# Optimization experiments

Measured on AMD Instinct MI355X. Metric: run time of the kernel, lower is better.

Reference implementation:

```python
import jax, jax.numpy as jnp
import numpy as np

N = 100_000      # nodes
E = 3_200_000    # edges (before self-loops)
IN_DIM = 256
H1, H2 = 64, 32
OUT_DIM = 40
NEG_SLOPE = 0.2  # PyG GATConv default


def setup_inputs() -> dict:
    key = jax.random.key(0)
    ks = jax.random.split(key, 12)
    s = 0.05
    return {
        "x": jax.random.normal(ks[0], (N, IN_DIM), jnp.float32),
        "edge_index": jax.random.randint(ks[1], (2, E), 0, N, jnp.int32),
        "W1": jax.random.normal(ks[2], (IN_DIM, H1), jnp.float32) * s,
        "att_src1": jax.random.normal(ks[3], (H1,), jnp.float32) * s,
        "att_dst1": jax.random.normal(ks[4], (H1,), jnp.float32) * s,
        "b1": jnp.zeros((H1,), jnp.float32),
        "W2": jax.random.normal(ks[5], (H1, H2), jnp.float32) * s,
        "att_src2": jax.random.normal(ks[6], (H2,), jnp.float32) * s,
        "att_dst2": jax.random.normal(ks[7], (H2,), jnp.float32) * s,
        "b2": jnp.zeros((H2,), jnp.float32),
        "fcW": jax.random.normal(ks[8], (H2, OUT_DIM), jnp.float32) * s,
        "fcb": jnp.zeros((OUT_DIM,), jnp.float32),
    }


def gat_conv(x, src, dst, W, a_src, a_dst, b):
    """Single-head PyG GATConv (concat, heads=1). src/dst already include self-loops."""
    n = x.shape[0]
    h = x @ W                                   # [N, C] projected features (lin has no bias)
    alpha_s = (h * a_src).sum(-1)               # [N]
    alpha_d = (h * a_dst).sum(-1)               # [N]
    logit = jax.nn.leaky_relu(alpha_s[src] + alpha_d[dst], NEG_SLOPE)  # [E']
    # segment softmax over edges grouped by destination node
    m = jax.ops.segment_max(logit, dst, num_segments=n)               # [N]
    e = jnp.exp(logit - m[dst])                                        # [E']
    denom = jax.ops.segment_sum(e, dst, num_segments=n)               # [N]
    alpha = e / denom[dst]                                             # [E']
    out = jax.ops.segment_sum(h[src] * alpha[:, None], dst, num_segments=n)  # [N, C]
    return out + b


def reference(x, edge_index, W1, att_src1, att_dst1, b1, W2, att_src2, att_dst2, b2, fcW, fcb):
    n = x.shape[0]
    # add_self_loops=True (PyG GATConv default)
    loop = jnp.arange(n, dtype=edge_index.dtype)
    src = jnp.concatenate([edge_index[0], loop])
    dst = jnp.concatenate([edge_index[1], loop])
    h = jax.nn.relu(gat_conv(x, src, dst, W1, att_src1, att_dst1, b1))
    emb = jax.nn.relu(gat_conv(h, src, dst, W2, att_src2, att_dst2, b2))
    logits = emb @ fcW + fcb
    return emb, logits
```

## Files before the change

### kernel.cpp

```cpp
#include <hip/hip_runtime.h>
#include <hip/hip_bf16.h>

#define NEG_SLOPE 0.2f
#define IN_DIM 256
#define C1 64
#define C2 32
#define ODIM 40
#define SCAN_CHUNK 4096
#define BSHIFT 12
#define ECHUNK 8192
#define ECH2 16384
#define CH 10

typedef unsigned short ushort16;

__device__ __forceinline__ unsigned bf16_rne(float f) {
    unsigned a = __float_as_uint(f);
    return (a + 0x7FFFu + ((a >> 16) & 1u)) >> 16;
}
__device__ __forceinline__ void bf16x2_unpack(unsigned u, float& f0, float& f1) {
    f0 = __uint_as_float(u << 16);
    f1 = __uint_as_float(u & 0xFFFF0000u);
}


__global__ void k_bhist(const int* __restrict__ dst, int E, int* __restrict__ gh,
                        int nblk, int nb) {
    __shared__ int h[32];
    int t = threadIdx.x;
    if (t < 32) h[t] = 0;
    __syncthreads();
    int base = blockIdx.x * ECHUNK;
    int end = min(base + ECHUNK, E);
    for (int i = base + t; i < end; i += 256) atomicAdd(&h[dst[i] >> BSHIFT], 1);
    __syncthreads();
    if (t < nb) gh[t * nblk + blockIdx.x] = h[t];
}

__global__ void k_bscan(int* __restrict__ gh, int L) {
    __shared__ int lds[256];
    __shared__ int carry;
    int t = threadIdx.x;
    if (t == 0) carry = 0;
    __syncthreads();
    for (int base = 0; base < L; base += 256) {
        int v = (base + t < L) ? gh[base + t] : 0;
        lds[t] = v; __syncthreads();
        for (int off = 1; off < 256; off <<= 1) {
            int u = (t >= off) ? lds[t - off] : 0;
            __syncthreads();
            lds[t] += u;
            __syncthreads();
        }
        if (base + t < L) gh[base + t] = lds[t] - v + carry;
        __syncthreads();
        if (t == 0) carry += lds[255];
        __syncthreads();
    }
}

__global__ void k_bplace(const int* __restrict__ src, const int* __restrict__ dst, int E,
                         const int* __restrict__ gh, int nblk, int nb,
                         int2* __restrict__ pairs) {
    __shared__ int cur[32];
    int t = threadIdx.x;
    if (t < nb) cur[t] = gh[t * nblk + blockIdx.x];
    __syncthreads();
    int base = blockIdx.x * ECHUNK;
    int end = min(base + ECHUNK, E);
    for (int i = base + t; i < end; i += 256) {
        int d = dst[i];
        int pos = atomicAdd(&cur[d >> BSHIFT], 1);
        pairs[pos] = make_int2(src[i], d);
    }
}

__device__ __forceinline__ void bc_map(int blk, int* b, int* c) {
    int xcd = blk & 7, k = blk >> 3;
    *b = (k & 3) * 8 + xcd;
    *c = k >> 2;
}

__global__ __launch_bounds__(512)
void k_nhist(const int2* __restrict__ pairs, const int* __restrict__ gh, int nblk,
             int nb, int E, int* __restrict__ chist) {
    __shared__ int h[4096];
    int b, c; bc_map(blockIdx.x, &b, &c);
    if (b >= nb) return;
    for (int i = threadIdx.x; i < 4096; i += 512) h[i] = 0;
    __syncthreads();
    int estart = gh[b * nblk];
    int eend = (b + 1 < nb) ? gh[(b + 1) * nblk] : E;
    int s0 = estart + c * ECH2;
    int s1 = min(s0 + ECH2, eend);
    for (int i = s0 + threadIdx.x; i < s1; i += 512)
        atomicAdd(&h[pairs[i].y & 4095], 1);
    __syncthreads();
    int* out = chist + ((size_t)b * CH + c) * 4096;
    for (int i = threadIdx.x; i < 4096; i += 512) out[i] = h[i];
}

__global__ void k_cnt(const int* __restrict__ chist, int* __restrict__ cnt, int n) {
    int i = blockIdx.x * 256 + threadIdx.x;
    if (i >= n) return;
    int b = i >> BSHIFT, j = i & 4095;
    const int* p = chist + ((size_t)b * CH) * 4096 + j;
    int s = 1;
#pragma unroll
    for (int c = 0; c < CH; c++) s += p[c * 4096];
    cnt[i] = s;
}

__global__ void k_scan1(const int* __restrict__ cnt, int n, int* __restrict__ bsums) {
    __shared__ int lds[256];
    int t = threadIdx.x;
    int base = blockIdx.x * SCAN_CHUNK + t * 16;
    int s = 0;
#pragma unroll
    for (int i = 0; i < 16; i++) { int idx = base + i; s += (idx < n) ? cnt[idx] : 0; }
    lds[t] = s; __syncthreads();
    for (int off = 128; off > 0; off >>= 1) {
        if (t < off) lds[t] += lds[t + off];
        __syncthreads();
    }
    if (t == 0) bsums[blockIdx.x] = lds[0];
}

__global__ void k_scan2(int* bsums, int nb, int* row_ptr, int n, int total) {
    __shared__ int lds[256];
    int t = threadIdx.x;
    int v = (t < nb) ? bsums[t] : 0;
    lds[t] = v; __syncthreads();
    for (int off = 1; off < 256; off <<= 1) {
        int u = (t >= off) ? lds[t - off] : 0;
        __syncthreads();
        lds[t] += u;
        __syncthreads();
    }
    if (t < nb) bsums[t] = lds[t] - v;
    if (t == 0) row_ptr[n] = total;
}

__global__ void k_scan3(const int* __restrict__ cnt, int n, const int* __restrict__ bsums,
                        int* __restrict__ row_ptr) {
    __shared__ int lds[256];
    int t = threadIdx.x;
    int base = blockIdx.x * SCAN_CHUNK + t * 16;
    int loc[16];
    int s = 0;
#pragma unroll
    for (int i = 0; i < 16; i++) {
        int idx = base + i;
        int c = (idx < n) ? cnt[idx] : 0;
        loc[i] = s; s += c;
    }
    lds[t] = s; __syncthreads();
    for (int off = 1; off < 256; off <<= 1) {
        int u = (t >= off) ? lds[t - off] : 0;
        __syncthreads();
        lds[t] += u;
        __syncthreads();
    }
    int texcl = lds[t] - s + bsums[blockIdx.x];
#pragma unroll
    for (int i = 0; i < 16; i++) {
        int idx = base + i;
        if (idx < n) row_ptr[idx] = texcl + loc[i];
    }
}

__global__ void k_selfloop(const int* __restrict__ row_ptr, int n, int* __restrict__ adj) {
    int i = blockIdx.x * 256 + threadIdx.x;
    if (i < n) adj[row_ptr[i]] = i;
}

__global__ void k_nscan(int* __restrict__ chist, const int* __restrict__ row_ptr, int n) {
    int i = blockIdx.x * 256 + threadIdx.x;
    if (i >= n) return;
    int b = i >> BSHIFT, j = i & 4095;
    int* p = chist + ((size_t)b * CH) * 4096 + j;
    int s = row_ptr[i] + 1;
#pragma unroll
    for (int c = 0; c < CH; c++) { int t = p[c * 4096]; p[c * 4096] = s; s += t; }
}

__global__ __launch_bounds__(512)
void k_place2(const int2* __restrict__ pairs, const int* __restrict__ gh, int nblk,
              int nb, int E, const int* __restrict__ chist, int* __restrict__ adj) {
    __shared__ int cur[4096];
    int b, c; bc_map(blockIdx.x, &b, &c);
    if (b >= nb) return;
    const int* cs = chist + ((size_t)b * CH + c) * 4096;
    for (int i = threadIdx.x; i < 4096; i += 512) cur[i] = cs[i];
    __syncthreads();
    int estart = gh[b * nblk];
    int eend = (b + 1 < nb) ? gh[(b + 1) * nblk] : E;
    int s0 = estart + c * ECH2;
    int s1 = min(s0 + ECH2, eend);
    for (int i = s0 + threadIdx.x; i < s1; i += 512) {
        int2 p = pairs[i];
        int pos = atomicAdd(&cur[p.y & 4095], 1);
        adj[pos] = p.x;
    }
}


__global__ __launch_bounds__(256, 4)
void k_gemm1(const float* __restrict__ x, const float* __restrict__ W1,
             const float* __restrict__ attS, const float* __restrict__ attD,
             ushort16* __restrict__ h1b, float* __restrict__ asP,
             float* __restrict__ adP, int n) {
    int t = threadIdx.x;
    int wave = t >> 6, lane = t & 63;
    int half = blockIdx.x & 1;
    int chalf = half * 32;
    int row = (blockIdx.x >> 1) * 256 + wave * 64 + lane;
    bool active = row < n;
    int rowc = active ? row : n - 1;
    const float4* xr = (const float4*)(x + (size_t)rowc * IN_DIM);

    float acc[32];
#pragma unroll
    for (int c = 0; c < 32; c++) acc[c] = 0.f;

#define FMA_K(XC, KK) { \
        const float* wk = wb + (KK) * C1; \
        _Pragma("unroll") \
        for (int c = 0; c < 32; c++) acc[c] = fmaf((XC), wk[c], acc[c]); }

    for (int k0 = 0; k0 < 16; k0++) {
        float4 xv0 = xr[k0 * 4 + 0];
        float4 xv1 = xr[k0 * 4 + 1];
        float4 xv2 = xr[k0 * 4 + 2];
        float4 xv3 = xr[k0 * 4 + 3];
        const float* wb = W1 + (size_t)(k0 * 16) * C1 + chalf;
        FMA_K(xv0.x, 0)  FMA_K(xv0.y, 1)  FMA_K(xv0.z, 2)  FMA_K(xv0.w, 3)
        FMA_K(xv1.x, 4)  FMA_K(xv1.y, 5)  FMA_K(xv1.z, 6)  FMA_K(xv1.w, 7)
        FMA_K(xv2.x, 8)  FMA_K(xv2.y, 9)  FMA_K(xv2.z, 10) FMA_K(xv2.w, 11)
        FMA_K(xv3.x, 12) FMA_K(xv3.y, 13) FMA_K(xv3.z, 14) FMA_K(xv3.w, 15)
    }
#undef FMA_K

    if (!active) return;
    float vs = 0.f, vd = 0.f;
#pragma unroll
    for (int c = 0; c < 32; c++) {
        vs = fmaf(acc[c], attS[chalf + c], vs);
        vd = fmaf(acc[c], attD[chalf + c], vd);
    }
    asP[half * n + row] = vs;
    adP[half * n + row] = vd;

    uint4* hp = (uint4*)((ushort16*)h1b + (size_t)row * C1 + chalf);
#pragma unroll
    for (int j = 0; j < 4; j++) {
        unsigned p0 = bf16_rne(acc[j*8+0]) | (bf16_rne(acc[j*8+1]) << 16);
        unsigned p1 = bf16_rne(acc[j*8+2]) | (bf16_rne(acc[j*8+3]) << 16);
        unsigned p2 = bf16_rne(acc[j*8+4]) | (bf16_rne(acc[j*8+5]) << 16);
        unsigned p3 = bf16_rne(acc[j*8+6]) | (bf16_rne(acc[j*8+7]) << 16);
        hp[j] = make_uint4(p0, p1, p2, p3);
    }
}

__global__ void k_alphaC(const float* __restrict__ asP, const float* __restrict__ adP,
                         float* __restrict__ as1, float* __restrict__ ad1, int n) {
    int i = blockIdx.x * 256 + threadIdx.x;
    if (i < n) {
        as1[i] = asP[i] + asP[(size_t)n + i];
        ad1[i] = adP[i] + adP[(size_t)n + i];
    }
}


__global__ __launch_bounds__(256)
void k_agg1(const ushort16* __restrict__ h1b, const float* __restrict__ as1,
            const float* __restrict__ ad1, const int* __restrict__ row_ptr,
            const int* __restrict__ adj, const float* __restrict__ b1,
            float* __restrict__ h1out, int n) {
    int wave = (blockIdx.x * 256 + threadIdx.x) >> 6;
    int lane = threadIdx.x & 63;
    if (wave >= n) return;
    int d = wave;
    int beg = row_ptr[d], end = row_ptr[d + 1];
    float adv = ad1[d];
    int g = lane >> 3, cq = lane & 7;
    float acc[8];
#pragma unroll
    for (int k = 0; k < 8; k++) acc[k] = 0.f;
    float dsum = 0.f;

#define AGG1_ROUND(E_) { \
        int se = __shfl(s, (E_)); \
        float we = __shfl(w, (E_)); \
        uint4 u = ((const uint4*)(h1b + (size_t)se * C1))[cq]; \
        float f0, f1; \
        bf16x2_unpack(u.x, f0, f1); acc[0]=fmaf(we,f0,acc[0]); acc[1]=fmaf(we,f1,acc[1]); \
        bf16x2_unpack(u.y, f0, f1); acc[2]=fmaf(we,f0,acc[2]); acc[3]=fmaf(we,f1,acc[3]); \
        bf16x2_unpack(u.z, f0, f1); acc[4]=fmaf(we,f0,acc[4]); acc[5]=fmaf(we,f1,acc[5]); \
        bf16x2_unpack(u.w, f0, f1); acc[6]=fmaf(we,f0,acc[6]); acc[7]=fmaf(we,f1,acc[7]); }

    for (int base = beg; base < end; base += 64) {
        int cnt = min(64, end - base);
        int s = d; float w = 0.f;
        if (lane < cnt) {
            s = adj[base + lane];
            float lg = as1[s] + adv;
            lg = lg > 0.f ? lg : NEG_SLOPE * lg;
            w = expf(lg);
            dsum += w;
        }
        int j = 0;
        for (; j + 32 <= cnt; j += 32) {
            AGG1_ROUND(j + g)
            AGG1_ROUND(j + 8 + g)
            AGG1_ROUND(j + 16 + g)
            AGG1_ROUND(j + 24 + g)
        }
        for (; j < cnt; j += 8) AGG1_ROUND(j + g)
    }
#undef AGG1_ROUND

#pragma unroll
    for (int off = 32; off > 0; off >>= 1) dsum += __shfl_xor(dsum, off);
#pragma unroll
    for (int off = 8; off <= 32; off <<= 1) {
#pragma unroll
        for (int k = 0; k < 8; k++) acc[k] += __shfl_xor(acc[k], off);
    }
    if (g == 0) {
        float inv = 1.f / dsum;
        float4 bv0 = ((const float4*)b1)[cq * 2];
        float4 bv1 = ((const float4*)b1)[cq * 2 + 1];
        float4 o0, o1;
        o0.x = acc[0] * inv + bv0.x; o0.x = o0.x > 0.f ? o0.x : 0.f;
        o0.y = acc[1] * inv + bv0.y; o0.y = o0.y > 0.f ? o0.y : 0.f;
        o0.z = acc[2] * inv + bv0.z; o0.z = o0.z > 0.f ? o0.z : 0.f;
        o0.w = acc[3] * inv + bv0.w; o0.w = o0.w > 0.f ? o0.w : 0.f;
        o1.x = acc[4] * inv + bv1.x; o1.x = o1.x > 0.f ? o1.x : 0.f;
        o1.y = acc[5] * inv + bv1.y; o1.y = o1.y > 0.f ? o1.y : 0.f;
        o1.z = acc[6] * inv + bv1.z; o1.z = o1.z > 0.f ? o1.z : 0.f;
        o1.w = acc[7] * inv + bv1.w; o1.w = o1.w > 0.f ? o1.w : 0.f;
        float4* op = (float4*)(h1out + (size_t)d * C1 + cq * 8);
        op[0] = o0; op[1] = o1;
    }
}


__global__ __launch_bounds__(256)
void k_gemm2(const float* __restrict__ h1out, const float* __restrict__ W2,
             const float* __restrict__ attS, const float* __restrict__ attD,
             ushort16* __restrict__ h2b, float* __restrict__ as2,
             float* __restrict__ ad2, int n) {
    __shared__ float w2t[C2 * 68];
    __shared__ float sAttS[C2], sAttD[C2];
    int t = threadIdx.x;
    for (int i = t; i < C1 * C2; i += 256) {
        int k = i >> 5, c = i & 31;
        w2t[c * 68 + k] = W2[i];
    }
    if (t < C2) { sAttS[t] = attS[t]; sAttD[t] = attD[t]; }
    __syncthreads();
    int wave = t >> 6, lane = t & 63;
    int col = lane & 31, half = lane >> 5;
    int rowbase = blockIdx.x * 32 + wave * 8;
    const float* wrow = &w2t[col * 68];
    for (int rr = 0; rr < 8; rr += 2) {
        int row = rowbase + rr + half;
        if (row >= n) return;
        float acc = 0.f;
#pragma unroll
        for (int k = 0; k < C1; k += 4) {
            float4 wv = *(const float4*)&wrow[k];
            float4 xv = *(const float4*)&h1out[(size_t)row * C1 + k];
            acc = fmaf(xv.x, wv.x, acc);
            acc = fmaf(xv.y, wv.y, acc);
            acc = fmaf(xv.z, wv.z, acc);
            acc = fmaf(xv.w, wv.w, acc);
        }
        h2b[(size_t)row * C2 + col] = (ushort16)bf16_rne(acc);
        float vs = acc * sAttS[col], vd = acc * sAttD[col];
#pragma unroll
        for (int off = 16; off > 0; off >>= 1) {
            vs += __shfl_xor(vs, off);
            vd += __shfl_xor(vd, off);
        }
        if (col == 0) { as2[row] = vs; ad2[row] = vd; }
    }
}


__global__ __launch_bounds__(256)
void k_agg2(const ushort16* __restrict__ h2b, const float* __restrict__ as2,
            const float* __restrict__ ad2, const int* __restrict__ row_ptr,
            const int* __restrict__ adj, const float* __restrict__ b2,
            float* __restrict__ emb, int n) {
    int wave = (blockIdx.x * 256 + threadIdx.x) >> 6;
    int lane = threadIdx.x & 63;
    if (wave >= n) return;
    int d = wave;
    int beg = row_ptr[d], end = row_ptr[d + 1];
    float adv = ad2[d];
    int g = lane >> 2, cq = lane & 3;
    float acc[8];
#pragma unroll
    for (int k = 0; k < 8; k++) acc[k] = 0.f;
    float dsum = 0.f;

#define AGG2_ROUND(E_) { \
        int se = __shfl(s, (E_)); \
        float we = __shfl(w, (E_)); \
        uint4 u = ((const uint4*)(h2b + (size_t)se * C2))[cq]; \
        float f0, f1; \
        bf16x2_unpack(u.x, f0, f1); acc[0]=fmaf(we,f0,acc[0]); acc[1]=fmaf(we,f1,acc[1]); \
        bf16x2_unpack(u.y, f0, f1); acc[2]=fmaf(we,f0,acc[2]); acc[3]=fmaf(we,f1,acc[3]); \
        bf16x2_unpack(u.z, f0, f1); acc[4]=fmaf(we,f0,acc[4]); acc[5]=fmaf(we,f1,acc[5]); \
        bf16x2_unpack(u.w, f0, f1); acc[6]=fmaf(we,f0,acc[6]); acc[7]=fmaf(we,f1,acc[7]); }

    for (int base = beg; base < end; base += 64) {
        int cnt = min(64, end - base);
        int s = d; float w = 0.f;
        if (lane < cnt) {
            s = adj[base + lane];
            float lg = as2[s] + adv;
            lg = lg > 0.f ? lg : NEG_SLOPE * lg;
            w = expf(lg);
            dsum += w;
        }
        int j = 0;
        for (; j + 64 <= cnt; j += 64) {
            AGG2_ROUND(j + g)
            AGG2_ROUND(j + 16 + g)
            AGG2_ROUND(j + 32 + g)
            AGG2_ROUND(j + 48 + g)
        }
        for (; j < cnt; j += 16) AGG2_ROUND(j + g)
    }
#undef AGG2_ROUND

#pragma unroll
    for (int off = 32; off > 0; off >>= 1) dsum += __shfl_xor(dsum, off);
#pragma unroll
    for (int off = 4; off <= 32; off <<= 1) {
#pragma unroll
        for (int k = 0; k < 8; k++) acc[k] += __shfl_xor(acc[k], off);
    }
    if (g == 0) {
        float inv = 1.f / dsum;
        float4 bv0 = ((const float4*)b2)[cq * 2];
        float4 bv1 = ((const float4*)b2)[cq * 2 + 1];
        float4 o0, o1;
        o0.x = acc[0] * inv + bv0.x; o0.x = o0.x > 0.f ? o0.x : 0.f;
        o0.y = acc[1] * inv + bv0.y; o0.y = o0.y > 0.f ? o0.y : 0.f;
        o0.z = acc[2] * inv + bv0.z; o0.z = o0.z > 0.f ? o0.z : 0.f;
        o0.w = acc[3] * inv + bv0.w; o0.w = o0.w > 0.f ? o0.w : 0.f;
        o1.x = acc[4] * inv + bv1.x; o1.x = o1.x > 0.f ? o1.x : 0.f;
        o1.y = acc[5] * inv + bv1.y; o1.y = o1.y > 0.f ? o1.y : 0.f;
        o1.z = acc[6] * inv + bv1.z; o1.z = o1.z > 0.f ? o1.z : 0.f;
        o1.w = acc[7] * inv + bv1.w; o1.w = o1.w > 0.f ? o1.w : 0.f;
        float4* op = (float4*)(emb + (size_t)d * C2 + cq * 8);
        op[0] = o0; op[1] = o1;
    }
}


__global__ __launch_bounds__(256)
void k_logits(const float* __restrict__ emb, const float* __restrict__ fcW,
              const float* __restrict__ fcb, float* __restrict__ out, int n) {
    __shared__ float w[C2 * ODIM];
    __shared__ float b[ODIM];
    int t = threadIdx.x;
    for (int i = t; i < C2 * ODIM; i += 256) w[i] = fcW[i];
    if (t < ODIM) b[t] = fcb[t];
    __syncthreads();
    int lane = t & 63;
    int row = blockIdx.x * 4 + (t >> 6);
    if (row >= n) return;
    float acc = (lane < ODIM) ? b[lane] : 0.f;
    const float4* er = (const float4*)&emb[(size_t)row * C2];
#pragma unroll
    for (int c4 = 0; c4 < 8; c4++) {
        float4 e = er[c4];
        int c = c4 * 4;
        if (lane < ODIM) {
            acc = fmaf(e.x, w[(c + 0) * ODIM + lane], acc);
            acc = fmaf(e.y, w[(c + 1) * ODIM + lane], acc);
            acc = fmaf(e.z, w[(c + 2) * ODIM + lane], acc);
            acc = fmaf(e.w, w[(c + 3) * ODIM + lane], acc);
        }
    }
    if (lane < ODIM) out[(size_t)row * ODIM + lane] = acc;
}


extern "C" void kernel_launch(void* const* d_in, const int* in_sizes, int n_in,
                              void* d_out, int out_size, void* d_ws, size_t ws_size,
                              hipStream_t stream) {
    const float* x    = (const float*)d_in[0];
    const int*   ei   = (const int*)d_in[1];
    const float* W1   = (const float*)d_in[2];
    const float* aS1  = (const float*)d_in[3];
    const float* aD1  = (const float*)d_in[4];
    const float* b1   = (const float*)d_in[5];
    const float* W2   = (const float*)d_in[6];
    const float* aS2  = (const float*)d_in[7];
    const float* aD2  = (const float*)d_in[8];
    const float* b2   = (const float*)d_in[9];
    const float* fcW  = (const float*)d_in[10];
    const float* fcb  = (const float*)d_in[11];

    const int N = in_sizes[0] / IN_DIM;
    const int E = in_sizes[1] / 2;
    const int* src = ei;
    const int* dst = ei + E;

    ushort16* h1b = (ushort16*)d_ws;
    float* h1out  = (float*)((char*)d_ws + (size_t)N * C1 * 2);
    float* as1    = h1out + (size_t)N * C1;
    float* ad1    = as1 + N;
    float* as2    = ad1 + N;
    float* ad2    = as2 + N;
    float* asP    = ad2 + N;
    float* adP    = asP + 2 * (size_t)N;
    int*   cnt    = (int*)(adP + 2 * (size_t)N);
    int*   row_ptr = cnt + N;
    int*   bsums   = row_ptr + (N + 1);
    int*   adj     = bsums + 256;
    int*   gh      = adj + (E + N);

    int2* pairs = (int2*)h1out;
    int*  chist = (int*)h1b;
    ushort16* h2b = (ushort16*)h1b;

    float* emb    = (float*)d_out;
    float* logits = emb + (size_t)N * C2;

    int nbN   = (N + 255) / 256;
    int nbS   = (N + SCAN_CHUNK - 1) / SCAN_CHUNK;
    int nblkE = (E + ECHUNK - 1) / ECHUNK;
    int nb    = (N + (1 << BSHIFT) - 1) >> BSHIFT;
    int nBC   = 8 * 4 * CH;

    k_bhist<<<nblkE, 256, 0, stream>>>(dst, E, gh, nblkE, nb);
    k_bscan<<<1, 256, 0, stream>>>(gh, nb * nblkE);
    k_bplace<<<nblkE, 256, 0, stream>>>(src, dst, E, gh, nblkE, nb, pairs);
    k_nhist<<<nBC, 512, 0, stream>>>(pairs, gh, nblkE, nb, E, chist);
    k_cnt<<<nbN, 256, 0, stream>>>(chist, cnt, N);
    k_scan1<<<nbS, 256, 0, stream>>>(cnt, N, bsums);
    k_scan2<<<1, 256, 0, stream>>>(bsums, nbS, row_ptr, N, E + N);
    k_scan3<<<nbS, 256, 0, stream>>>(cnt, N, bsums, row_ptr);
    k_selfloop<<<nbN, 256, 0, stream>>>(row_ptr, N, adj);
    k_nscan<<<nbN, 256, 0, stream>>>(chist, row_ptr, N);
    k_place2<<<nBC, 512, 0, stream>>>(pairs, gh, nblkE, nb, E, chist, adj);

    int nbG1 = 2 * ((N + 255) / 256);
    k_gemm1<<<nbG1, 256, 0, stream>>>(x, W1, aS1, aD1, h1b, asP, adP, N);
    k_alphaC<<<nbN, 256, 0, stream>>>(asP, adP, as1, ad1, N);
    int nbA = (N + 3) / 4;
    k_agg1<<<nbA, 256, 0, stream>>>(h1b, as1, ad1, row_ptr, adj, b1, h1out, N);
    int nbG2 = (N + 31) / 32;
    k_gemm2<<<nbG2, 256, 0, stream>>>(h1out, W2, aS2, aD2, h2b, as2, ad2, N);
    k_agg2<<<nbA, 256, 0, stream>>>(h2b, as2, ad2, row_ptr, adj, b2, emb, N);
    k_logits<<<nbA, 256, 0, stream>>>(emb, fcW, fcb, logits, N);
}
```

Measured before the change: 410.0 us.

## Pack bucketed edge pairs into 32-bit words and stage scatter through LDS

```diff
diff --git a/kernel.cpp b/kernel.cpp
--- a/kernel.cpp
+++ b/kernel.cpp
@@ -11,6 +11,7 @@
 #define ECHUNK 8192
 #define ECH2 16384
 #define CH 10
+#define SRCMASK 0x1FFFF
 
 typedef unsigned short ushort16;
 
@@ -59,19 +60,42 @@
     }
 }
 
-__global__ void k_bplace(const int* __restrict__ src, const int* __restrict__ dst, int E,
-                         const int* __restrict__ gh, int nblk, int nb,
-                         int2* __restrict__ pairs) {
-    __shared__ int cur[32];
-    int t = threadIdx.x;
-    if (t < nb) cur[t] = gh[t * nblk + blockIdx.x];
+__global__ __launch_bounds__(256)
+void k_bplace(const int* __restrict__ src, const int* __restrict__ dst, int E,
+              const int* __restrict__ gh, int nblk, int nb,
+              unsigned* __restrict__ pairs) {
+    __shared__ int cnt32[32], lofs[33], lcur[32], delta[32];
+    __shared__ unsigned buf[ECHUNK];
+    int t = threadIdx.x;
+    if (t < 32) cnt32[t] = 0;
     __syncthreads();
     int base = blockIdx.x * ECHUNK;
     int end = min(base + ECHUNK, E);
+    for (int i = base + t; i < end; i += 256) atomicAdd(&cnt32[dst[i] >> BSHIFT], 1);
+    __syncthreads();
+    if (t == 0) {
+        int s = 0;
+        for (int b = 0; b < 32; b++) { lofs[b] = s; s += cnt32[b]; }
+        lofs[32] = s;
+    }
+    __syncthreads();
+    if (t < 32) {
+        lcur[t] = lofs[t];
+        delta[t] = (t < nb) ? (gh[t * nblk + blockIdx.x] - lofs[t]) : 0;
+    }
+    __syncthreads();
     for (int i = base + t; i < end; i += 256) {
         int d = dst[i];
-        int pos = atomicAdd(&cur[d >> BSHIFT], 1);
-        pairs[pos] = make_int2(src[i], d);
+        int b = d >> BSHIFT;
+        int p = atomicAdd(&lcur[b], 1);
+        buf[p] = (unsigned)src[i] | ((unsigned)(d & 4095) << 17);
+    }
+    __syncthreads();
+    int m = end - base;
+    for (int j = t; j < m; j += 256) {
+        int lo = 0, hi = 31;
+        while (lo < hi) { int mid = (lo + hi + 1) >> 1; if (lofs[mid] <= j) lo = mid; else hi = mid - 1; }
+        pairs[j + delta[lo]] = buf[j];
     }
 }
 
@@ -82,7 +106,7 @@
 }
 
 __global__ __launch_bounds__(512)
-void k_nhist(const int2* __restrict__ pairs, const int* __restrict__ gh, int nblk,
+void k_nhist(const unsigned* __restrict__ pairs, const int* __restrict__ gh, int nblk,
              int nb, int E, int* __restrict__ chist) {
     __shared__ int h[4096];
     int b, c; bc_map(blockIdx.x, &b, &c);
@@ -94,7 +118,7 @@
     int s0 = estart + c * ECH2;
     int s1 = min(s0 + ECH2, eend);
     for (int i = s0 + threadIdx.x; i < s1; i += 512)
-        atomicAdd(&h[pairs[i].y & 4095], 1);
+        atomicAdd(&h[(pairs[i] >> 17) & 4095], 1);
     __syncthreads();
     int* out = chist + ((size_t)b * CH + c) * 4096;
     for (int i = threadIdx.x; i < 4096; i += 512) out[i] = h[i];
@@ -185,8 +209,9 @@
 }
 
 __global__ __launch_bounds__(512)
-void k_place2(const int2* __restrict__ pairs, const int* __restrict__ gh, int nblk,
-              int nb, int E, const int* __restrict__ chist, int* __restrict__ adj) {
+void k_place2(const unsigned* __restrict__ pairs, const int* __restrict__ gh, int nblk,
+              int nb, int E, const int* __restrict__ chist, int* __restrict__ adj,
+              int bbase) {
     __shared__ int cur[4096];
     int b, c; bc_map(blockIdx.x, &b, &c);
     if (b >= nb) return;
@@ -197,10 +222,11 @@
     int eend = (b + 1 < nb) ? gh[(b + 1) * nblk] : E;
     int s0 = estart + c * ECH2;
     int s1 = min(s0 + ECH2, eend);
+    int nbase = b << BSHIFT; (void)nbase; (void)bbase;
     for (int i = s0 + threadIdx.x; i < s1; i += 512) {
-        int2 p = pairs[i];
-        int pos = atomicAdd(&cur[p.y & 4095], 1);
-        adj[pos] = p.x;
+        unsigned p = pairs[i];
+        int pos = atomicAdd(&cur[(p >> 17) & 4095], 1);
+        adj[pos] = (int)(p & SRCMASK);
     }
 }
 
@@ -527,7 +553,7 @@
     int*   adj     = bsums + 256;
     int*   gh      = adj + (E + N);
 
-    int2* pairs = (int2*)h1out;
+    unsigned* pairs = (unsigned*)h1out;
     int*  chist = (int*)h1b;
     ushort16* h2b = (ushort16*)h1b;
 
@@ -550,7 +576,7 @@
     k_scan3<<<nbS, 256, 0, stream>>>(cnt, N, bsums, row_ptr);
     k_selfloop<<<nbN, 256, 0, stream>>>(row_ptr, N, adj);
     k_nscan<<<nbN, 256, 0, stream>>>(chist, row_ptr, N);
-    k_place2<<<nBC, 512, 0, stream>>>(pairs, gh, nblkE, nb, E, chist, adj);
+    k_place2<<<nBC, 512, 0, stream>>>(pairs, gh, nblkE, nb, E, chist, adj, 0);
 
     int nbG1 = 2 * ((N + 255) / 256);
     k_gemm1<<<nbG1, 256, 0, stream>>>(x, W1, aS1, aD1, h1b, asP, adP, N);
```

Result: slower. 421.8 us (+2.9%).
